# Optimization experiments

Hardware: AMD Instinct MI355X
Metric: run time of the kernel (lower is better)

## Reference

```python
import jax, jax.numpy as jnp
import numpy as np

B, S, D, HD = 4, 4096, 1024, 64

def setup_inputs() -> dict:
    key = jax.random.key(0)
    ks = jax.random.split(key, 4)
    scale = 1.0 / np.sqrt(D)
    return {
        "x": jax.random.normal(ks[0], (B, S, D), dtype=jnp.float32),
        "wq": jax.random.normal(ks[1], (HD, D), dtype=jnp.float32) * scale,
        "bq": jnp.zeros((HD,), dtype=jnp.float32),
        "wk": jax.random.normal(ks[2], (HD, D), dtype=jnp.float32) * scale,
        "bk": jnp.zeros((HD,), dtype=jnp.float32),
        "wv": jax.random.normal(ks[3], (HD, D), dtype=jnp.float32) * scale,
        "bv": jnp.zeros((HD,), dtype=jnp.float32),
    }

def reference(x, wq, bq, wk, bk, wv, bv):
    seq_len = x.shape[1]
    head_dim = wq.shape[0]
    # projections: nn.Linear stores weight as [out, in]
    q = jnp.einsum('bsd,hd->bsh', x, wq) + bq  # [B,S,HD]
    k = jnp.einsum('bsd,hd->bsh', x, wk) + bk
    v = jnp.einsum('bsd,hd->bsh', x, wv) + bv
    score = jnp.einsum('bqh,bkh->bqk', q, k) / jnp.sqrt(jnp.float32(head_dim))  # [B,S,S]
    causal = jnp.tril(jnp.ones((seq_len, seq_len), dtype=bool))
    score = jnp.where(causal, score, -jnp.inf)
    attn = jax.nn.softmax(score, axis=-1)
    # dropout p=0.0 -> identity
    out = jnp.einsum('bqk,bkh->bqh', attn, v)  # [B,S,HD]
    return out
```

## Files before the change

### kernel.cpp

```cpp
#include <hip/hip_runtime.h>
#include <math.h>

#define B_   4
#define S_   4096
#define D_   1024
#define HD_  64

#define CK            8
#define CHUNKS_PER_B  288
#define FULL_CHUNKS   224
#define PSTRIDE       68
#define SLOT_F        (64 * PSTRIDE)

#define QSCALE   (0.125f * 1.44269504089f)

typedef float  f32x4  __attribute__((ext_vector_type(4)));
typedef __bf16 bf16x8 __attribute__((ext_vector_type(8)));
typedef __bf16 bf16x4 __attribute__((ext_vector_type(4)));

static __device__ __forceinline__ unsigned short bfbits(float f) {
    __bf16 h = (__bf16)f;
    return __builtin_bit_cast(unsigned short, h);
}

static __device__ __forceinline__ float exp2_hw(float x) {
    return __builtin_exp2f(x);
}

static __device__ __forceinline__ int chunk_slot(int qi, int c) {
    const int a = qi >> 3, r = qi & 7;
    return qi + 4 * a * (a - 1) + a * r + c;
}

__global__ __launch_bounds__(256) void convert_w(
    const float* __restrict__ wq, const float* __restrict__ wk,
    const float* __restrict__ wv, unsigned short* __restrict__ wbf)
{
    const int col = blockIdx.x;
    const int p = col >> 6, h = col & 63;
    const float* src = (p == 0 ? wq : (p == 1 ? wk : wv)) + (size_t)h * D_;
    const int t = threadIdx.x;
    const float4 v = ((const float4*)src)[t];
    bf16x4 o;
    o[0] = (__bf16)v.x; o[1] = (__bf16)v.y; o[2] = (__bf16)v.z; o[3] = (__bf16)v.w;
    *(bf16x4*)&wbf[(size_t)col * D_ + 4 * t] = o;
}

__global__ __launch_bounds__(256) void proj_mfma(
    const float* __restrict__ x, const unsigned short* __restrict__ wbf,
    const float* __restrict__ bq, const float* __restrict__ bk,
    const float* __restrict__ bv,
    unsigned short* __restrict__ qbf, unsigned short* __restrict__ kbf,
    unsigned short* __restrict__ vtb)
{
    __shared__ unsigned short xs[32][136];
    __shared__ unsigned short wsh[96][136];

    const int t = threadIdx.x;
    const int w = t >> 6, lane = t & 63;
    const int n = lane & 15, g = lane >> 4;
    const int koff = 8 * g;
    const int rt = w & 1, cg = w >> 1;
    const size_t row0 = (size_t)blockIdx.x * 32;
    const int colbase = 96 * blockIdx.y;

    f32x4 acc[3];
#pragma unroll
    for (int i = 0; i < 3; ++i) acc[i] = (f32x4)0.f;

    for (int chunk = 0; chunk < 8; ++chunk) {
        const int d0 = chunk * 128;
        __syncthreads();
#pragma unroll
        for (int i = 0; i < 4; ++i) {
            int e = t + i * 256;
            int r = e >> 5, c4 = (e & 31) * 4;
            float4 v = *(const float4*)&x[(row0 + r) * D_ + d0 + c4];
            bf16x4 o;
            o[0] = (__bf16)v.x; o[1] = (__bf16)v.y;
            o[2] = (__bf16)v.z; o[3] = (__bf16)v.w;
            *(bf16x4*)&xs[r][c4] = o;
        }
#pragma unroll
        for (int i = 0; i < 6; ++i) {
            int e = t + i * 256;
            int col = e >> 4, g8 = (e & 15) * 8;
            uint4 v = *(const uint4*)&wbf[(size_t)(colbase + col) * D_ + d0 + g8];
            *(uint4*)&wsh[col][g8] = v;
        }
        __syncthreads();

#pragma unroll
        for (int ks = 0; ks < 4; ++ks) {
            const int k0 = 32 * ks;
            const bf16x8 a = *(const bf16x8*)&xs[16 * rt + n][k0 + koff];
#pragma unroll
            for (int ci = 0; ci < 3; ++ci) {
                const bf16x8 b = *(const bf16x8*)&wsh[48 * cg + 16 * ci + n][k0 + koff];
                acc[ci] = __builtin_amdgcn_mfma_f32_16x16x32_bf16(a, b, acc[ci], 0, 0, 0);
            }
        }
    }

#pragma unroll
    for (int ci = 0; ci < 3; ++ci) {
        const int gct = 6 * blockIdx.y + 3 * cg + ci;
        const int p = gct >> 2, h0 = (gct & 3) * 16;
        const int h = h0 + n;
        const float bb = (p == 0 ? bq : (p == 1 ? bk : bv))[h];
        if (p == 2) {
            const size_t grow0 = row0 + 16 * rt + 4 * g;
            const int bidx = (int)(grow0 >> 12);
            const int s0 = (int)(grow0 & 4095);
            bf16x4 u;
            u[0] = (__bf16)(acc[ci][0] + bb); u[1] = (__bf16)(acc[ci][1] + bb);
            u[2] = (__bf16)(acc[ci][2] + bb); u[3] = (__bf16)(acc[ci][3] + bb);
            *(bf16x4*)&vtb[((size_t)bidx * HD_ + h) * S_ + s0] = u;
        } else {
            unsigned short* outp = (p == 0 ? qbf : kbf);
            const float scale = (p == 0) ? QSCALE : 1.0f;
#pragma unroll
            for (int r = 0; r < 4; ++r) {
                const size_t grow = row0 + 16 * rt + 4 * g + r;
                outp[grow * HD_ + h] = bfbits((acc[ci][r] + bb) * scale);
            }
        }
    }
}

__global__ __launch_bounds__(256) void flash_splitk(
    const unsigned short* __restrict__ qg, const unsigned short* __restrict__ kg,
    const unsigned short* __restrict__ vt, float* __restrict__ out,
    float* __restrict__ part)
{
    __shared__ unsigned short qsh[64][72];
    __shared__ unsigned short ksh[64][72];
    __shared__ unsigned short vsh[64][72];
    __shared__ unsigned short psh[4][16][72];

    const int t    = threadIdx.x;
    const int w    = t >> 6;
    const int lane = t & 63;
    const int n    = lane & 15;
    const int g    = lane >> 4;
    const int koff = 8 * g;

    int b, qi, c;
    {
        const int idx = blockIdx.x;
        if (idx < B_ * FULL_CHUNKS) {
            b = idx / FULL_CHUNKS;
            int rem = idx - b * FULL_CHUNKS;
            qi = 8;
            while (rem >= (qi >> 3)) { rem -= (qi >> 3); ++qi; }
            c = rem;
        } else {
            const int r2 = idx - B_ * FULL_CHUNKS;
            b = r2 >> 6;
            qi = r2 & 63;
            c = qi >> 3;
        }
    }
    const int kt0 = c * CK;
    const int kt1 = min(qi, kt0 + CK - 1);
    const int nc  = (qi >> 3) + 1;

    const size_t qtile = ((size_t)b * S_ + (size_t)qi * 64) * HD_;

    {
        const uint4* src = (const uint4*)(qg + qtile);
#pragma unroll
        for (int i = 0; i < 2; ++i) {
            int e = t + i * 256;
            int r = e >> 3, gg = e & 7;
            *(uint4*)&qsh[r][8 * gg] = src[e];
        }
    }

    f32x4 o4[4];
#pragma unroll
    for (int i = 0; i < 4; ++i) o4[i] = (f32x4)0.f;
    float m_r = -INFINITY, l_r = 0.f;

    for (int kt = kt0; kt <= kt1; ++kt) {
        const size_t kvbase = ((size_t)b * S_ + (size_t)kt * 64) * HD_;
        __syncthreads();
        {
            const uint4* ksrc = (const uint4*)(kg + kvbase);
#pragma unroll
            for (int i = 0; i < 2; ++i) {
                int e = t + i * 256;
                int r = e >> 3, gg = e & 7;
                *(uint4*)&ksh[r][8 * gg] = ksrc[e];
            }
#pragma unroll
            for (int i = 0; i < 2; ++i) {
                int e = t + i * 256;
                int h = e >> 3, gg = e & 7;
                *(uint4*)&vsh[h][8 * gg] =
                    *(const uint4*)&vt[((size_t)b * HD_ + h) * S_ + kt * 64 + 8 * gg];
            }
        }
        __syncthreads();

        f32x4 sc[4];
#pragma unroll
        for (int mt = 0; mt < 4; ++mt) sc[mt] = (f32x4)0.f;
#pragma unroll
        for (int ks = 0; ks < 2; ++ks) {
            const bf16x8 bq8 = *(const bf16x8*)&qsh[16 * w + n][32 * ks + koff];
#pragma unroll
            for (int mt = 0; mt < 4; ++mt) {
                const bf16x8 ak = *(const bf16x8*)&ksh[16 * mt + n][32 * ks + koff];
                sc[mt] = __builtin_amdgcn_mfma_f32_16x16x32_bf16(ak, bq8, sc[mt], 0, 0, 0);
            }
        }

        if (kt == qi) {
            const int qloc = 16 * w + n;
#pragma unroll
            for (int mt = 0; mt < 4; ++mt)
#pragma unroll
                for (int r = 0; r < 4; ++r) {
                    const int kloc = 16 * mt + 4 * g + r;
                    if (kloc > qloc) sc[mt][r] = -INFINITY;
                }
        }

        float mx = -INFINITY;
#pragma unroll
        for (int mt = 0; mt < 4; ++mt)
#pragma unroll
            for (int r = 0; r < 4; ++r) mx = fmaxf(mx, sc[mt][r]);
        mx = fmaxf(mx, __shfl_xor(mx, 16));
        mx = fmaxf(mx, __shfl_xor(mx, 32));

        const float m_new = fmaxf(m_r, mx);
        const float alpha = exp2_hw(m_r - m_new);
        float psum = 0.f;
#pragma unroll
        for (int mt = 0; mt < 4; ++mt)
#pragma unroll
            for (int r = 0; r < 4; ++r) {
                const float pe = exp2_hw(sc[mt][r] - m_new);
                sc[mt][r] = pe;
                psum += pe;
            }
        psum += __shfl_xor(psum, 16);
        psum += __shfl_xor(psum, 32);
        l_r = l_r * alpha + psum;
        m_r = m_new;

#pragma unroll
        for (int ht = 0; ht < 4; ++ht)
#pragma unroll
            for (int r = 0; r < 4; ++r) o4[ht][r] *= alpha;

#pragma unroll
        for (int mt = 0; mt < 4; ++mt) {
            bf16x4 u;
            u[0] = (__bf16)sc[mt][0]; u[1] = (__bf16)sc[mt][1];
            u[2] = (__bf16)sc[mt][2]; u[3] = (__bf16)sc[mt][3];
            *(bf16x4*)&psh[w][n][16 * mt + 4 * g] = u;
        }

#pragma unroll
        for (int ks = 0; ks < 2; ++ks) {
            const bf16x8 ap = *(const bf16x8*)&psh[w][n][32 * ks + koff];
#pragma unroll
            for (int ht = 0; ht < 4; ++ht) {
                const bf16x8 av = *(const bf16x8*)&vsh[16 * ht + n][32 * ks + koff];
                o4[ht] = __builtin_amdgcn_mfma_f32_16x16x32_bf16(av, ap, o4[ht], 0, 0, 0);
            }
        }
    }

    const size_t qbase = ((size_t)b * S_ + (size_t)qi * 64) * HD_;
    if (nc == 1) {
        const float inv = 1.f / l_r;
        const size_t ob = qbase + (size_t)(16 * w + n) * HD_;
#pragma unroll
        for (int ht = 0; ht < 4; ++ht) {
            float4 rv;
            rv.x = o4[ht][0] * inv; rv.y = o4[ht][1] * inv;
            rv.z = o4[ht][2] * inv; rv.w = o4[ht][3] * inv;
            *(float4*)&out[ob + 16 * ht + 4 * g] = rv;
        }
    } else {
        const size_t sb = ((size_t)b * CHUNKS_PER_B + chunk_slot(qi, c)) * SLOT_F;
        const size_t pb = sb + (size_t)(16 * w + n) * PSTRIDE;
#pragma unroll
        for (int ht = 0; ht < 4; ++ht) {
            float4 rv;
            rv.x = o4[ht][0]; rv.y = o4[ht][1];
            rv.z = o4[ht][2]; rv.w = o4[ht][3];
            *(float4*)&part[pb + 16 * ht + 4 * g] = rv;
        }
        if (g == 0) {
            part[pb + 64] = m_r;
            part[pb + 65] = l_r;
        }
    }
}

__global__ __launch_bounds__(256) void combine(
    const float* __restrict__ part, float* __restrict__ out)
{
    const int t  = threadIdx.x;
    const int qr = t >> 2, tc = t & 3;
    const int qi = blockIdx.x + CK;
    const int b  = blockIdx.y;
    const int nc = (qi >> 3) + 1;

    const size_t base0 = ((size_t)b * CHUNKS_PER_B + chunk_slot(qi, 0)) * SLOT_F;

    float M = -INFINITY;
    for (int c0 = 0; c0 < nc; ++c0)
        M = fmaxf(M, part[base0 + (size_t)c0 * SLOT_F + qr * PSTRIDE + 64]);

    float L = 0.f;
    float o[16];
#pragma unroll
    for (int j = 0; j < 16; ++j) o[j] = 0.f;

    for (int c0 = 0; c0 < nc; ++c0) {
        const size_t sb = base0 + (size_t)c0 * SLOT_F + qr * PSTRIDE;
        const float m_c = part[sb + 64];
        const float l_c = part[sb + 65];
        const float w = exp2_hw(m_c - M);
        L += w * l_c;
#pragma unroll
        for (int j = 0; j < 4; ++j) {
            const float4 ov = *(const float4*)&part[sb + tc * 16 + 4 * j];
            o[4 * j + 0] += w * ov.x; o[4 * j + 1] += w * ov.y;
            o[4 * j + 2] += w * ov.z; o[4 * j + 3] += w * ov.w;
        }
    }

    const float inv = 1.f / L;
    const size_t qbase = ((size_t)b * S_ + (size_t)qi * 64) * HD_;
#pragma unroll
    for (int j = 0; j < 4; ++j) {
        float4 r;
        r.x = o[4 * j + 0] * inv; r.y = o[4 * j + 1] * inv;
        r.z = o[4 * j + 2] * inv; r.w = o[4 * j + 3] * inv;
        *(float4*)&out[qbase + 16 * t + 4 * j] = r;
    }
}

extern "C" void kernel_launch(void* const* d_in, const int* in_sizes, int n_in,
                              void* d_out, int out_size, void* d_ws, size_t ws_size,
                              hipStream_t stream)
{
    const float* x  = (const float*)d_in[0];
    const float* wq = (const float*)d_in[1];
    const float* bq = (const float*)d_in[2];
    const float* wk = (const float*)d_in[3];
    const float* bk = (const float*)d_in[4];
    const float* wv = (const float*)d_in[5];
    const float* bv = (const float*)d_in[6];
    float* outp = (float*)d_out;

    const size_t n = (size_t)B_ * S_ * HD_;
    unsigned short* qbf = (unsigned short*)d_ws;
    unsigned short* kbf = qbf + n;
    unsigned short* vtb = kbf + n;
    unsigned short* wbf = vtb + n;
    float* part = (float*)(wbf + (size_t)192 * D_);

    convert_w<<<dim3(192), 256, 0, stream>>>(wq, wk, wv, wbf);
    proj_mfma<<<dim3(B_ * S_ / 32, 2), 256, 0, stream>>>(
        x, wbf, bq, bk, bv, qbf, kbf, vtb);
    flash_splitk<<<dim3(B_ * CHUNKS_PER_B), 256, 0, stream>>>(
        qbf, kbf, vtb, outp, part);
    combine<<<dim3(S_ / 64 - CK, B_), 256, 0, stream>>>(part, outp);
}
```

Before: 156.5 us.

## Store split-K partial outputs in bf16 and split combine across head-dim quarters

The split-K flash kernel now writes its unnormalized partial outputs as bf16 instead of fp32, keeping m and l as fp32 packed into the row padding. This halves the partial-buffer traffic between the attention and combine kernels. The combine kernel gains a third grid dimension of four, so each thread reduces 4 head-dim values instead of 16, giving more parallelism and fewer registers per thread. Rounding unnormalized accumulators to bf16 before the rescale-and-sum adds precision loss to the output.

Measured after the change: 153.0 us. -2.3%, faster.

```diff
diff --git a/kernel.cpp b/kernel.cpp
--- a/kernel.cpp
+++ b/kernel.cpp
@@ -9,8 +9,8 @@
 #define CK            8
 #define CHUNKS_PER_B  288
 #define FULL_CHUNKS   224
-#define PSTRIDE       68
-#define SLOT_F        (64 * PSTRIDE)
+#define PSTRIDE_SH    72
+#define SLOT_SH       (64 * PSTRIDE_SH)
 
 #define QSCALE   (0.125f * 1.44269504089f)
 
@@ -131,7 +131,7 @@
 __global__ __launch_bounds__(256) void flash_splitk(
     const unsigned short* __restrict__ qg, const unsigned short* __restrict__ kg,
     const unsigned short* __restrict__ vt, float* __restrict__ out,
-    float* __restrict__ part)
+    unsigned short* __restrict__ part)
 {
     __shared__ unsigned short qsh[64][72];
     __shared__ unsigned short ksh[64][72];
@@ -287,65 +287,62 @@
             *(float4*)&out[ob + 16 * ht + 4 * g] = rv;
         }
     } else {
-        const size_t sb = ((size_t)b * CHUNKS_PER_B + chunk_slot(qi, c)) * SLOT_F;
-        const size_t pb = sb + (size_t)(16 * w + n) * PSTRIDE;
+        const size_t sb = ((size_t)b * CHUNKS_PER_B + chunk_slot(qi, c)) * SLOT_SH;
+        const size_t pb = sb + (size_t)(16 * w + n) * PSTRIDE_SH;
 #pragma unroll
         for (int ht = 0; ht < 4; ++ht) {
-            float4 rv;
-            rv.x = o4[ht][0]; rv.y = o4[ht][1];
-            rv.z = o4[ht][2]; rv.w = o4[ht][3];
-            *(float4*)&part[pb + 16 * ht + 4 * g] = rv;
+            bf16x4 u;
+            u[0] = (__bf16)o4[ht][0]; u[1] = (__bf16)o4[ht][1];
+            u[2] = (__bf16)o4[ht][2]; u[3] = (__bf16)o4[ht][3];
+            *(bf16x4*)&part[pb + 16 * ht + 4 * g] = u;
         }
         if (g == 0) {
-            part[pb + 64] = m_r;
-            part[pb + 65] = l_r;
+            *(float*)&part[pb + 64] = m_r;
+            *(float*)&part[pb + 66] = l_r;
         }
     }
 }
 
 __global__ __launch_bounds__(256) void combine(
-    const float* __restrict__ part, float* __restrict__ out)
+    const unsigned short* __restrict__ part, float* __restrict__ out)
 {
     const int t  = threadIdx.x;
     const int qr = t >> 2, tc = t & 3;
     const int qi = blockIdx.x + CK;
     const int b  = blockIdx.y;
+    const int hq = blockIdx.z;
     const int nc = (qi >> 3) + 1;
 
-    const size_t base0 = ((size_t)b * CHUNKS_PER_B + chunk_slot(qi, 0)) * SLOT_F;
+    const size_t base0 = ((size_t)b * CHUNKS_PER_B + chunk_slot(qi, 0)) * SLOT_SH
+                       + (size_t)qr * PSTRIDE_SH;
 
     float M = -INFINITY;
     for (int c0 = 0; c0 < nc; ++c0)
-        M = fmaxf(M, part[base0 + (size_t)c0 * SLOT_F + qr * PSTRIDE + 64]);
+        M = fmaxf(M, *(const float*)&part[base0 + (size_t)c0 * SLOT_SH + 64]);
 
     float L = 0.f;
-    float o[16];
-#pragma unroll
-    for (int j = 0; j < 16; ++j) o[j] = 0.f;
+    float o[4];
+#pragma unroll
+    for (int j = 0; j < 4; ++j) o[j] = 0.f;
+
+    const int ho = hq * 16 + tc * 4;
 
     for (int c0 = 0; c0 < nc; ++c0) {
-        const size_t sb = base0 + (size_t)c0 * SLOT_F + qr * PSTRIDE;
-        const float m_c = part[sb + 64];
-        const float l_c = part[sb + 65];
+        const size_t sb = base0 + (size_t)c0 * SLOT_SH;
+        const float m_c = *(const float*)&part[sb + 64];
+        const float l_c = *(const float*)&part[sb + 66];
         const float w = exp2_hw(m_c - M);
         L += w * l_c;
-#pragma unroll
-        for (int j = 0; j < 4; ++j) {
-            const float4 ov = *(const float4*)&part[sb + tc * 16 + 4 * j];
-            o[4 * j + 0] += w * ov.x; o[4 * j + 1] += w * ov.y;
-            o[4 * j + 2] += w * ov.z; o[4 * j + 3] += w * ov.w;
-        }
+        const bf16x4 ov = *(const bf16x4*)&part[sb + ho];
+#pragma unroll
+        for (int j = 0; j < 4; ++j) o[j] += w * (float)ov[j];
     }
 
     const float inv = 1.f / L;
-    const size_t qbase = ((size_t)b * S_ + (size_t)qi * 64) * HD_;
-#pragma unroll
-    for (int j = 0; j < 4; ++j) {
-        float4 r;
-        r.x = o[4 * j + 0] * inv; r.y = o[4 * j + 1] * inv;
-        r.z = o[4 * j + 2] * inv; r.w = o[4 * j + 3] * inv;
-        *(float4*)&out[qbase + 16 * t + 4 * j] = r;
-    }
+    const size_t ob = ((size_t)b * S_ + (size_t)qi * 64 + qr) * HD_ + ho;
+    float4 r;
+    r.x = o[0] * inv; r.y = o[1] * inv; r.z = o[2] * inv; r.w = o[3] * inv;
+    *(float4*)&out[ob] = r;
 }
 
 extern "C" void kernel_launch(void* const* d_in, const int* in_sizes, int n_in,
@@ -366,12 +363,12 @@
     unsigned short* kbf = qbf + n;
     unsigned short* vtb = kbf + n;
     unsigned short* wbf = vtb + n;
-    float* part = (float*)(wbf + (size_t)192 * D_);
+    unsigned short* part = wbf + (size_t)192 * D_;
 
     convert_w<<<dim3(192), 256, 0, stream>>>(wq, wk, wv, wbf);
     proj_mfma<<<dim3(B_ * S_ / 32, 2), 256, 0, stream>>>(
         x, wbf, bq, bk, bv, qbf, kbf, vtb);
     flash_splitk<<<dim3(B_ * CHUNKS_PER_B), 256, 0, stream>>>(
         qbf, kbf, vtb, outp, part);
-    combine<<<dim3(S_ / 64 - CK, B_), 256, 0, stream>>>(part, outp);
-}
+    combine<<<dim3(S_ / 64 - CK, B_, 4), 256, 0, stream>>>(part, outp);
+}
```
